# Performance work log

Measured on AMD Instinct MI355X. Metric: run time of the kernel, lower is better.

## Reference

```python
import jax, jax.numpy as jnp
import numpy as np


def setup_inputs() -> dict:
    key = jax.random.key(0)
    k1, k2, k3, k4, k5 = jax.random.split(key, 5)
    B, S, DK, D = 64, 2048, 1024, 1024
    hidden_state = jax.random.normal(k1, (B, D), dtype=jnp.float32)
    encoder_outputs = jax.random.normal(k2, (B, S, DK), dtype=jnp.float32)
    # linear1: in = dim_key + dim*num_layers = 2048, out = dim = 1024
    W1 = jax.random.normal(k3, (D, DK + D), dtype=jnp.float32) * (1.0 / np.sqrt(DK + D))
    b1 = jax.random.normal(k4, (D,), dtype=jnp.float32) * 0.01
    W2 = jax.random.normal(k5, (1, D), dtype=jnp.float32) * (1.0 / np.sqrt(D))
    return {"hidden_state": hidden_state, "encoder_outputs": encoder_outputs,
            "W1": W1, "b1": b1, "W2": W2}


def reference(hidden_state, encoder_outputs, W1, b1, W2):
    # torch: cat([enc, h], -1) @ W1.T  ==  enc @ W1e.T + h @ W1h.T
    # (split avoids materializing the [B,S,DK+D] concat; same math)
    DK = encoder_outputs.shape[-1]
    W1e, W1h = W1[:, :DK], W1[:, DK:]
    # pre: [B, S, D]
    pre = (jnp.einsum('bsk,dk->bsd', encoder_outputs, W1e)
           + jnp.einsum('bm,dm->bd', hidden_state, W1h)[:, None, :]
           + b1)
    e = jnp.einsum('bsd,d->bs', jnp.tanh(pre), W2[0])  # scores [B, S]
    alpha = jax.nn.softmax(e, axis=1)
    context = jnp.einsum('bs,bsk->bk', alpha, encoder_outputs)  # [B, DK]
    return context
```

## Files before the change

kernel.cpp:

```cpp
#include <hip/hip_runtime.h>

typedef __attribute__((ext_vector_type(8))) short short8;
typedef __attribute__((ext_vector_type(4))) float floatx4;

#define M_TOT 131072
#define SEQ   2048
#define NB    8

__device__ __forceinline__ unsigned bf16rne(float x) {
  unsigned u = __float_as_uint(x);
  return (u + 0x7FFFu + ((u >> 16) & 1u)) >> 16;
}

#define GLOAD_LDS16(g, l) __builtin_amdgcn_global_load_lds( \
    (const __attribute__((address_space(1))) unsigned int*)(g), \
    (__attribute__((address_space(3))) unsigned int*)(l), 16, 0, 0)

__global__ __launch_bounds__(256) void convert_enc_kernel(
    const float* __restrict__ in, unsigned int* __restrict__ out)
{
  size_t i = ((size_t)blockIdx.x * 256 + threadIdx.x) * 8;
  float4 a = *(const float4*)(in + i);
  float4 b = *(const float4*)(in + i + 4);
  uint4 o;
  o.x = bf16rne(a.x) | (bf16rne(a.y) << 16);
  o.y = bf16rne(a.z) | (bf16rne(a.w) << 16);
  o.z = bf16rne(b.x) | (bf16rne(b.y) << 16);
  o.w = bf16rne(b.z) | (bf16rne(b.w) << 16);
  *(uint4*)(out + i / 2) = o;
}

__global__ __launch_bounds__(128) void convert_w1e_kernel(
    const float* __restrict__ W1, unsigned int* __restrict__ out)
{
  int d = blockIdx.x;
  int k = threadIdx.x * 8;
  const float* p = W1 + (size_t)d * 2048 + k;
  float4 a = *(const float4*)p;
  float4 b = *(const float4*)(p + 4);
  uint4 o;
  o.x = bf16rne(a.x) | (bf16rne(a.y) << 16);
  o.y = bf16rne(a.z) | (bf16rne(a.w) << 16);
  o.z = bf16rne(b.x) | (bf16rne(b.y) << 16);
  o.w = bf16rne(b.z) | (bf16rne(b.w) << 16);
  *(uint4*)(out + ((size_t)d * 1024 + k) / 2) = o;
}

__global__ __launch_bounds__(256) void hvec_kernel(
    const float* __restrict__ hid, const float* __restrict__ W1,
    const float* __restrict__ b1, float* __restrict__ hvec)
{
  int b = blockIdx.x, g = blockIdx.y;
  int w = threadIdx.x >> 6, lane = threadIdx.x & 63;
  const float* hrow = hid + b * 1024;
  for (int i = 0; i < 16; ++i) {
    int d = g * 64 + w * 16 + i;
    const float* wrow = W1 + (size_t)d * 2048 + 1024;
    float sum = 0.f;
#pragma unroll
    for (int c = 0; c < 4; ++c) {
      int m = c * 256 + lane * 4;
      float4 wv = *(const float4*)(wrow + m);
      float4 hv = *(const float4*)(hrow + m);
      sum += wv.x * hv.x + wv.y * hv.y + wv.z * hv.z + wv.w * hv.w;
    }
#pragma unroll
    for (int msk = 1; msk < 64; msk <<= 1) sum += __shfl_xor(sum, msk);
    if (lane == 0) hvec[b * 1024 + d] = sum + b1[d];
  }
}

__global__ __launch_bounds__(256) void gemm_bf16_kernel(
    const unsigned short* __restrict__ A, const unsigned short* __restrict__ B,
    const float* __restrict__ W2, const float* __restrict__ hvec,
    float* __restrict__ epart)
{
  __shared__ __align__(16) unsigned short Ah[128 * 32];
  __shared__ __align__(16) unsigned short Bh[128 * 32];
  __shared__ float ep[2][128];

  const int tid = threadIdx.x;
  const int lid = blockIdx.x + blockIdx.y * 8;
  const int xcd = lid & 7;
  const int q   = lid >> 3;
  const int mb  = (xcd << 7) + (q >> 3);
  const int nb  = q & 7;
  const int r0 = mb * 128, n0 = nb * 128;
  const int bidx = r0 >> 11;
  const int w = tid >> 6, lane = tid & 63;
  const int wm = w >> 1, wn = w & 1;
  const int lrow = lane & 15, kq = lane >> 4;

  floatx4 acc[4][4];
#pragma unroll
  for (int i = 0; i < 4; ++i)
#pragma unroll
    for (int j = 0; j < 4; ++j)
      acc[i][j] = (floatx4){0.f, 0.f, 0.f, 0.f};

  const unsigned short* aBase = A + (size_t)r0 * 1024;
  const unsigned short* bBase = B + (size_t)n0 * 1024;

  for (int k0 = 0; k0 < 1024; k0 += 32) {
    __syncthreads();
#pragma unroll
    for (int j = 0; j < 2; ++j) {
      int c = tid + j * 256;
      int row = c >> 2, kc = c & 3;
      const unsigned short* ag = aBase + (size_t)row * 1024 + k0 + kc * 8;
      const unsigned short* bg = bBase + (size_t)row * 1024 + k0 + kc * 8;
      int ldsbase = (w * 64 + j * 256) * 8;
      GLOAD_LDS16(ag, &Ah[ldsbase]);
      GLOAD_LDS16(bg, &Bh[ldsbase]);
    }
    __syncthreads();

    short8 af[4], bfm[4];
#pragma unroll
    for (int t4 = 0; t4 < 4; ++t4) {
      af[t4]  = *(const short8*)&Ah[(wm * 64 + t4 * 16 + lrow) * 32 + kq * 8];
      bfm[t4] = *(const short8*)&Bh[(wn * 64 + t4 * 16 + lrow) * 32 + kq * 8];
    }
#pragma unroll
    for (int mt = 0; mt < 4; ++mt)
#pragma unroll
      for (int nt = 0; nt < 4; ++nt)
        acc[mt][nt] = __builtin_amdgcn_mfma_f32_16x16x32_bf16(
            af[mt], bfm[nt], acc[mt][nt], 0, 0, 0);
  }

  float hv[4], w2v[4];
#pragma unroll
  for (int nt = 0; nt < 4; ++nt) {
    int n = n0 + wn * 64 + nt * 16 + lrow;
    hv[nt]  = hvec[bidx * 1024 + n];
    w2v[nt] = W2[n];
  }
#pragma unroll
  for (int mt = 0; mt < 4; ++mt) {
#pragma unroll
    for (int r = 0; r < 4; ++r) {
      float sum = 0.f;
#pragma unroll
      for (int nt = 0; nt < 4; ++nt) {
        float pre = acc[mt][nt][r] + hv[nt];
        float ex = __expf(2.f * pre);
        sum += (1.f - 2.f / (ex + 1.f)) * w2v[nt];
      }
      sum += __shfl_xor(sum, 1);
      sum += __shfl_xor(sum, 2);
      sum += __shfl_xor(sum, 4);
      sum += __shfl_xor(sum, 8);
      if (lrow == 0) ep[wn][wm * 64 + mt * 16 + kq * 4 + r] = sum;
    }
  }
  __syncthreads();
  if (tid < 128)
    epart[(size_t)nb * M_TOT + r0 + tid] = ep[0][tid] + ep[1][tid];
}

__global__ __launch_bounds__(256) void fused_gemm_kernel(
    const float* __restrict__ enc, const float* __restrict__ W1,
    const float* __restrict__ W2, const float* __restrict__ hvec,
    float* __restrict__ epart)
{
  __shared__ __align__(16) unsigned short Ah[128 * 32];
  __shared__ __align__(16) unsigned short Bh[128 * 32];
  __shared__ float ep[2][128];

  const int tid = threadIdx.x;
  const int nb = blockIdx.x, mb = blockIdx.y;
  const int r0 = mb * 128, n0 = nb * 128;
  const int bidx = r0 >> 11;
  const int w = tid >> 6, lane = tid & 63;
  const int wm = w >> 1, wn = w & 1;
  const int lrow = lane & 15, kq = lane >> 4;

  floatx4 acc[4][4];
#pragma unroll
  for (int i = 0; i < 4; ++i)
#pragma unroll
    for (int j = 0; j < 4; ++j)
      acc[i][j] = (floatx4){0.f, 0.f, 0.f, 0.f};

  const int srow = tid >> 3;
  const int scol = (tid & 7) * 4;
  const float* aptr = enc + (size_t)(r0 + srow) * 1024 + scol;
  const float* bptr = W1  + (size_t)(n0 + srow) * 2048 + scol;

  for (int k0 = 0; k0 < 1024; k0 += 32) {
    float4 av[4], bv[4];
#pragma unroll
    for (int j = 0; j < 4; ++j) {
      av[j] = *(const float4*)(aptr + (size_t)(j * 32) * 1024 + k0);
      bv[j] = *(const float4*)(bptr + (size_t)(j * 32) * 2048 + k0);
    }
    __syncthreads();
#pragma unroll
    for (int j = 0; j < 4; ++j) {
      unsigned ax = __float_as_uint(av[j].x), ay = __float_as_uint(av[j].y);
      unsigned az = __float_as_uint(av[j].z), aw = __float_as_uint(av[j].w);
      unsigned a01 = __builtin_amdgcn_perm(ay, ax, 0x07060302u);
      unsigned a23 = __builtin_amdgcn_perm(aw, az, 0x07060302u);
      *(uint2*)&Ah[(tid + j * 256) * 4] = make_uint2(a01, a23);
      unsigned bx = __float_as_uint(bv[j].x), by = __float_as_uint(bv[j].y);
      unsigned bz = __float_as_uint(bv[j].z), bw = __float_as_uint(bv[j].w);
      unsigned b01 = __builtin_amdgcn_perm(by, bx, 0x07060302u);
      unsigned b23 = __builtin_amdgcn_perm(bw, bz, 0x07060302u);
      *(uint2*)&Bh[(tid + j * 256) * 4] = make_uint2(b01, b23);
    }
    __syncthreads();

    short8 af[4], bfm[4];
#pragma unroll
    for (int t4 = 0; t4 < 4; ++t4) {
      af[t4]  = *(const short8*)&Ah[(wm * 64 + t4 * 16 + lrow) * 32 + kq * 8];
      bfm[t4] = *(const short8*)&Bh[(wn * 64 + t4 * 16 + lrow) * 32 + kq * 8];
    }
#pragma unroll
    for (int mt = 0; mt < 4; ++mt)
#pragma unroll
      for (int nt = 0; nt < 4; ++nt)
        acc[mt][nt] = __builtin_amdgcn_mfma_f32_16x16x32_bf16(
            af[mt], bfm[nt], acc[mt][nt], 0, 0, 0);
  }

  float hv[4], w2v[4];
#pragma unroll
  for (int nt = 0; nt < 4; ++nt) {
    int n = n0 + wn * 64 + nt * 16 + lrow;
    hv[nt]  = hvec[bidx * 1024 + n];
    w2v[nt] = W2[n];
  }
#pragma unroll
  for (int mt = 0; mt < 4; ++mt) {
#pragma unroll
    for (int r = 0; r < 4; ++r) {
      float sum = 0.f;
#pragma unroll
      for (int nt = 0; nt < 4; ++nt) {
        float pre = acc[mt][nt][r] + hv[nt];
        float ex = __expf(2.f * pre);
        sum += (1.f - 2.f / (ex + 1.f)) * w2v[nt];
      }
      sum += __shfl_xor(sum, 1);
      sum += __shfl_xor(sum, 2);
      sum += __shfl_xor(sum, 4);
      sum += __shfl_xor(sum, 8);
      if (lrow == 0) ep[wn][wm * 64 + mt * 16 + kq * 4 + r] = sum;
    }
  }
  __syncthreads();
  if (tid < 128)
    epart[(size_t)nb * M_TOT + r0 + tid] = ep[0][tid] + ep[1][tid];
}

__global__ __launch_bounds__(256) void softmax_kernel(
    const float* __restrict__ epart, float* __restrict__ alpha)
{
  int b = blockIdx.x, t = threadIdx.x;
  __shared__ float redmax[4], redsum[4];
  float ev[8];
  float lmax = -1e30f;
#pragma unroll
  for (int j = 0; j < 8; ++j) {
    int s = t + j * 256;
    float sum = 0.f;
#pragma unroll
    for (int p = 0; p < 8; ++p) sum += epart[(size_t)p * M_TOT + b * SEQ + s];
    ev[j] = sum;
    lmax = fmaxf(lmax, sum);
  }
#pragma unroll
  for (int msk = 1; msk < 64; msk <<= 1) lmax = fmaxf(lmax, __shfl_xor(lmax, msk));
  if ((t & 63) == 0) redmax[t >> 6] = lmax;
  __syncthreads();
  float bmax = fmaxf(fmaxf(redmax[0], redmax[1]), fmaxf(redmax[2], redmax[3]));
  float lsum = 0.f;
#pragma unroll
  for (int j = 0; j < 8; ++j) { ev[j] = __expf(ev[j] - bmax); lsum += ev[j]; }
#pragma unroll
  for (int msk = 1; msk < 64; msk <<= 1) lsum += __shfl_xor(lsum, msk);
  if ((t & 63) == 0) redsum[t >> 6] = lsum;
  __syncthreads();
  float inv = 1.f / (redsum[0] + redsum[1] + redsum[2] + redsum[3]);
#pragma unroll
  for (int j = 0; j < 8; ++j) alpha[b * SEQ + t + j * 256] = ev[j] * inv;
}

__global__ __launch_bounds__(256) void context_bf16_kernel(
    const unsigned int* __restrict__ encB, const float* __restrict__ alpha,
    float* __restrict__ out)
{
  __shared__ float red[8][128];
  int b = blockIdx.x, kc = blockIdx.y, t = threadIdx.x;
  int kl = (t & 31) * 4;
  int strip = t >> 5;
  const unsigned int* ep = encB +
      (((size_t)b * SEQ + strip * 256) * 1024 + kc * 128 + kl) / 2;
  const float* ap = alpha + b * SEQ + strip * 256;
  float a0 = 0.f, a1 = 0.f, a2 = 0.f, a3 = 0.f;
#pragma unroll 4
  for (int s = 0; s < 256; ++s) {
    float a = ap[s];
    uint2 v = *(const uint2*)(ep + (size_t)s * 512);
    a0 += a * __uint_as_float(v.x << 16);
    a1 += a * __uint_as_float(v.x & 0xFFFF0000u);
    a2 += a * __uint_as_float(v.y << 16);
    a3 += a * __uint_as_float(v.y & 0xFFFF0000u);
  }
  red[strip][kl + 0] = a0;
  red[strip][kl + 1] = a1;
  red[strip][kl + 2] = a2;
  red[strip][kl + 3] = a3;
  __syncthreads();
  if (t < 128) {
    float s = 0.f;
#pragma unroll
    for (int j = 0; j < 8; ++j) s += red[j][t];
    out[b * 1024 + kc * 128 + t] = s;
  }
}

__global__ __launch_bounds__(256) void context_kernel(
    const float* __restrict__ enc, const float* __restrict__ alpha,
    float* __restrict__ out)
{
  int b = blockIdx.y, sq = blockIdx.z, t = threadIdx.x;
  int k4 = t * 4;
  const float* ep = enc + ((size_t)b * SEQ + sq * 128) * 1024 + k4;
  const float* ap = alpha + b * SEQ + sq * 128;
  float ax = 0.f, ay = 0.f, az = 0.f, aw = 0.f;
#pragma unroll 4
  for (int s = 0; s < 128; ++s) {
    float a = ap[s];
    float4 v = *(const float4*)(ep + (size_t)s * 1024);
    ax += a * v.x; ay += a * v.y; az += a * v.z; aw += a * v.w;
  }
  float* o = out + b * 1024 + k4;
  atomicAdd(o + 0, ax);
  atomicAdd(o + 1, ay);
  atomicAdd(o + 2, az);
  atomicAdd(o + 3, aw);
}

extern "C" void kernel_launch(void* const* d_in, const int* in_sizes, int n_in,
                              void* d_out, int out_size, void* d_ws, size_t ws_size,
                              hipStream_t stream) {
  const float* hid = (const float*)d_in[0];
  const float* enc = (const float*)d_in[1];
  const float* W1  = (const float*)d_in[2];
  const float* b1  = (const float*)d_in[3];
  const float* W2  = (const float*)d_in[4];
  float* out = (float*)d_out;

  float* epart = (float*)d_ws;
  float* alpha = epart + (size_t)NB * M_TOT;
  float* hvec  = alpha + M_TOT;
  size_t small_bytes = ((size_t)NB * M_TOT + M_TOT + 64 * 1024) * 4;
  size_t encB_off = ((small_bytes + 255) / 256) * 256;
  size_t need = encB_off + (size_t)M_TOT * 1024 * 2 + (size_t)1024 * 1024 * 2;

  hvec_kernel<<<dim3(64, 16), 256, 0, stream>>>(hid, W1, b1, hvec);

  if (ws_size >= need) {
    unsigned short* encB = (unsigned short*)((char*)d_ws + encB_off);
    unsigned short* W1eB = encB + (size_t)M_TOT * 1024;
    convert_enc_kernel<<<65536, 256, 0, stream>>>(enc, (unsigned int*)encB);
    convert_w1e_kernel<<<1024, 128, 0, stream>>>(W1, (unsigned int*)W1eB);
    gemm_bf16_kernel<<<dim3(NB, 1024), 256, 0, stream>>>(encB, W1eB, W2, hvec, epart);
    softmax_kernel<<<64, 256, 0, stream>>>(epart, alpha);
    context_bf16_kernel<<<dim3(64, 8), 256, 0, stream>>>((unsigned int*)encB, alpha, out);
  } else {
    hipMemsetAsync(d_out, 0, (size_t)out_size * sizeof(float), stream);
    fused_gemm_kernel<<<dim3(NB, 1024), 256, 0, stream>>>(enc, W1, W2, hvec, epart);
    softmax_kernel<<<64, 256, 0, stream>>>(epart, alpha);
    context_kernel<<<dim3(1, 64, 16), 256, 0, stream>>>(enc, alpha, out);
  }
}
```

Measured before the change: 1.157 ms.

## Use 256x256 bf16 GEMM tiles with 4-stage LDS pipeline and async prefetch

Replaces the 128x128 single-buffered bf16 GEMM with a 512-thread 256x256 tile kernel. It prefetches K-slices two steps ahead into a 4-deep LDS ring using global_load_lds, synchronises with explicit vmcnt waits plus barriers, and raises wave priority around the MFMA blocks. The larger tile halves the N-partials, so softmax is templated to sum 4 partials instead of 8. The aim is more data reuse per global load and overlap of memory latency with MFMA work. The cost is 128KB of LDS per block and higher register pressure with 2 blocks per CU requested.

```diff
diff --git a/kernel.cpp b/kernel.cpp
--- a/kernel.cpp
+++ b/kernel.cpp
@@ -70,65 +70,92 @@
   }
 }
 
-__global__ __launch_bounds__(256) void gemm_bf16_kernel(
+__global__ __launch_bounds__(512, 2) void gemm256_kernel(
     const unsigned short* __restrict__ A, const unsigned short* __restrict__ B,
     const float* __restrict__ W2, const float* __restrict__ hvec,
     float* __restrict__ epart)
 {
-  __shared__ __align__(16) unsigned short Ah[128 * 32];
-  __shared__ __align__(16) unsigned short Bh[128 * 32];
-  __shared__ float ep[2][128];
+  __shared__ __align__(16) unsigned short lds[4][2][8192];
 
   const int tid = threadIdx.x;
-  const int lid = blockIdx.x + blockIdx.y * 8;
-  const int xcd = lid & 7;
-  const int q   = lid >> 3;
-  const int mb  = (xcd << 7) + (q >> 3);
-  const int nb  = q & 7;
-  const int r0 = mb * 128, n0 = nb * 128;
+  const int lid = blockIdx.x;
+  const int xcd = lid & 7, q = lid >> 3;
+  const int mb = xcd * 64 + (q >> 2);
+  const int nb = q & 3;
+  const int r0 = mb * 256, n0 = nb * 256;
   const int bidx = r0 >> 11;
-  const int w = tid >> 6, lane = tid & 63;
-  const int wm = w >> 1, wn = w & 1;
+  const int wid = tid >> 6, lane = tid & 63;
+  const int wm = wid >> 2, wn = wid & 3;
   const int lrow = lane & 15, kq = lane >> 4;
 
-  floatx4 acc[4][4];
-#pragma unroll
-  for (int i = 0; i < 4; ++i)
+  int offA[2], offB[2], dst[2];
+#pragma unroll
+  for (int j = 0; j < 2; ++j) {
+    int c = tid + j * 512;
+    int r = c >> 2, s = c & 3;
+    offA[j] = (r0 + r) * 1024 + s * 8;
+    offB[j] = (n0 + r) * 1024 + s * 8;
+    dst[j] = (wid * 64 + j * 512) * 8;
+  }
+
+  floatx4 acc[8][4];
+#pragma unroll
+  for (int i = 0; i < 8; ++i)
 #pragma unroll
     for (int j = 0; j < 4; ++j)
       acc[i][j] = (floatx4){0.f, 0.f, 0.f, 0.f};
 
-  const unsigned short* aBase = A + (size_t)r0 * 1024;
-  const unsigned short* bBase = B + (size_t)n0 * 1024;
-
-  for (int k0 = 0; k0 < 1024; k0 += 32) {
-    __syncthreads();
-#pragma unroll
-    for (int j = 0; j < 2; ++j) {
-      int c = tid + j * 256;
-      int row = c >> 2, kc = c & 3;
-      const unsigned short* ag = aBase + (size_t)row * 1024 + k0 + kc * 8;
-      const unsigned short* bg = bBase + (size_t)row * 1024 + k0 + kc * 8;
-      int ldsbase = (w * 64 + j * 256) * 8;
-      GLOAD_LDS16(ag, &Ah[ldsbase]);
-      GLOAD_LDS16(bg, &Bh[ldsbase]);
-    }
-    __syncthreads();
-
-    short8 af[4], bfm[4];
-#pragma unroll
-    for (int t4 = 0; t4 < 4; ++t4) {
-      af[t4]  = *(const short8*)&Ah[(wm * 64 + t4 * 16 + lrow) * 32 + kq * 8];
-      bfm[t4] = *(const short8*)&Bh[(wn * 64 + t4 * 16 + lrow) * 32 + kq * 8];
-    }
-#pragma unroll
-    for (int mt = 0; mt < 4; ++mt)
-#pragma unroll
-      for (int nt = 0; nt < 4; ++nt)
-        acc[mt][nt] = __builtin_amdgcn_mfma_f32_16x16x32_bf16(
-            af[mt], bfm[nt], acc[mt][nt], 0, 0, 0);
-  }
-
+#define STAGE_J(T, J) do { \
+    GLOAD_LDS16(A + (size_t)offA[J] + (T) * 32, &lds[(T) & 3][0][dst[J]]); \
+    GLOAD_LDS16(B + (size_t)offB[J] + (T) * 32, &lds[(T) & 3][1][dst[J]]); \
+  } while (0)
+
+  STAGE_J(0, 0); STAGE_J(0, 1);
+  STAGE_J(1, 0); STAGE_J(1, 1);
+
+  const int aB = wm * 4096 + lrow * 32 + kq * 8;
+  const int bB = wn * 2048 + lrow * 32 + kq * 8;
+
+  for (int tt = 0; tt < 8; ++tt) {
+#pragma unroll
+    for (int u = 0; u < 4; ++u) {
+      const int t = tt * 4 + u;
+      const unsigned short* Ah = lds[u][0];
+      const unsigned short* Bh = lds[u][1];
+
+      if (t >= 30) { asm volatile("s_waitcnt vmcnt(0)" ::: "memory"); }
+      else         { asm volatile("s_waitcnt vmcnt(4)" ::: "memory"); }
+      __builtin_amdgcn_s_barrier();
+
+      short8 af[8];
+#pragma unroll
+      for (int mt = 0; mt < 8; ++mt) af[mt] = *(const short8*)&Ah[aB + mt * 512];
+      short8 bf0 = *(const short8*)&Bh[bB];
+      short8 bf1 = *(const short8*)&Bh[bB + 512];
+      if (t < 30) STAGE_J(t + 2, 0);
+      __builtin_amdgcn_s_setprio(1);
+#pragma unroll
+      for (int mt = 0; mt < 8; ++mt) {
+        acc[mt][0] = __builtin_amdgcn_mfma_f32_16x16x32_bf16(af[mt], bf0, acc[mt][0], 0, 0, 0);
+        acc[mt][1] = __builtin_amdgcn_mfma_f32_16x16x32_bf16(af[mt], bf1, acc[mt][1], 0, 0, 0);
+      }
+      __builtin_amdgcn_s_setprio(0);
+      short8 bf2 = *(const short8*)&Bh[bB + 1024];
+      short8 bf3 = *(const short8*)&Bh[bB + 1536];
+      if (t < 30) STAGE_J(t + 2, 1);
+      __builtin_amdgcn_s_setprio(1);
+#pragma unroll
+      for (int mt = 0; mt < 8; ++mt) {
+        acc[mt][2] = __builtin_amdgcn_mfma_f32_16x16x32_bf16(af[mt], bf2, acc[mt][2], 0, 0, 0);
+        acc[mt][3] = __builtin_amdgcn_mfma_f32_16x16x32_bf16(af[mt], bf3, acc[mt][3], 0, 0, 0);
+      }
+      __builtin_amdgcn_s_setprio(0);
+    }
+  }
+#undef STAGE_J
+
+  __syncthreads();
+  float* ep = (float*)&lds[0][0][0];
   float hv[4], w2v[4];
 #pragma unroll
   for (int nt = 0; nt < 4; ++nt) {
@@ -137,7 +164,7 @@
     w2v[nt] = W2[n];
   }
 #pragma unroll
-  for (int mt = 0; mt < 4; ++mt) {
+  for (int mt = 0; mt < 8; ++mt) {
 #pragma unroll
     for (int r = 0; r < 4; ++r) {
       float sum = 0.f;
@@ -151,12 +178,14 @@
       sum += __shfl_xor(sum, 2);
       sum += __shfl_xor(sum, 4);
       sum += __shfl_xor(sum, 8);
-      if (lrow == 0) ep[wn][wm * 64 + mt * 16 + kq * 4 + r] = sum;
-    }
-  }
-  __syncthreads();
-  if (tid < 128)
-    epart[(size_t)nb * M_TOT + r0 + tid] = ep[0][tid] + ep[1][tid];
+      if (lrow == 0) ep[wn * 256 + wm * 128 + mt * 16 + kq * 4 + r] = sum;
+    }
+  }
+  __syncthreads();
+  if (tid < 256) {
+    float s = ep[tid] + ep[256 + tid] + ep[512 + tid] + ep[768 + tid];
+    epart[(size_t)nb * M_TOT + r0 + tid] = s;
+  }
 }
 
 __global__ __launch_bounds__(256) void fused_gemm_kernel(
@@ -255,6 +284,7 @@
     epart[(size_t)nb * M_TOT + r0 + tid] = ep[0][tid] + ep[1][tid];
 }
 
+template<int NP>
 __global__ __launch_bounds__(256) void softmax_kernel(
     const float* __restrict__ epart, float* __restrict__ alpha)
 {
@@ -267,7 +297,7 @@
     int s = t + j * 256;
     float sum = 0.f;
 #pragma unroll
-    for (int p = 0; p < 8; ++p) sum += epart[(size_t)p * M_TOT + b * SEQ + s];
+    for (int p = 0; p < NP; ++p) sum += epart[(size_t)p * M_TOT + b * SEQ + s];
     ev[j] = sum;
     lmax = fmaxf(lmax, sum);
   }
@@ -368,13 +398,13 @@
     unsigned short* W1eB = encB + (size_t)M_TOT * 1024;
     convert_enc_kernel<<<65536, 256, 0, stream>>>(enc, (unsigned int*)encB);
     convert_w1e_kernel<<<1024, 128, 0, stream>>>(W1, (unsigned int*)W1eB);
-    gemm_bf16_kernel<<<dim3(NB, 1024), 256, 0, stream>>>(encB, W1eB, W2, hvec, epart);
-    softmax_kernel<<<64, 256, 0, stream>>>(epart, alpha);
+    gemm256_kernel<<<2048, 512, 0, stream>>>(encB, W1eB, W2, hvec, epart);
+    softmax_kernel<4><<<64, 256, 0, stream>>>(epart, alpha);
     context_bf16_kernel<<<dim3(64, 8), 256, 0, stream>>>((unsigned int*)encB, alpha, out);
   } else {
     hipMemsetAsync(d_out, 0, (size_t)out_size * sizeof(float), stream);
     fused_gemm_kernel<<<dim3(NB, 1024), 256, 0, stream>>>(enc, W1, W2, hvec, epart);
-    softmax_kernel<<<64, 256, 0, stream>>>(epart, alpha);
+    softmax_kernel<8><<<64, 256, 0, stream>>>(epart, alpha);
     context_kernel<<<dim3(1, 64, 16), 256, 0, stream>>>(enc, alpha, out);
   }
 }
```

Result: faster. 1.083 ms (-6.4%).

## Fuse encoder bf16 conversion into GEMM with pipelined fragment-layout W1 loads

Applied to the files above, without the earlier changes.

Removes the separate pass that converted the whole encoder tensor to bf16. The GEMM now loads fp32 encoder rows, converts them in registers with v_cvt_pk_bf16_f32 and stores them to double-buffered LDS. W1e is pre-packed into an MFMA fragment layout and prefetched into a 4-stage LDS ring, with manual waitcnt and setprio. The context pass reads fp32 encoder data directly with 512 threads, and hvec is spread over more blocks. This avoids writing and re-reading a 256MB bf16 copy, but the GEMM and the context pass now each read the full fp32 encoder tensor, and the GEMM does more per-thread conversion work.

```diff
diff --git a/kernel.cpp b/kernel.cpp
--- a/kernel.cpp
+++ b/kernel.cpp
@@ -12,30 +12,22 @@
   return (u + 0x7FFFu + ((u >> 16) & 1u)) >> 16;
 }
 
+__device__ __forceinline__ unsigned cvtpk_bf16(float lo, float hi) {
+  unsigned r;
+  asm("v_cvt_pk_bf16_f32 %0, %1, %2" : "=v"(r) : "v"(lo), "v"(hi));
+  return r;
+}
+
 #define GLOAD_LDS16(g, l) __builtin_amdgcn_global_load_lds( \
     (const __attribute__((address_space(1))) unsigned int*)(g), \
     (__attribute__((address_space(3))) unsigned int*)(l), 16, 0, 0)
 
-__global__ __launch_bounds__(256) void convert_enc_kernel(
-    const float* __restrict__ in, unsigned int* __restrict__ out)
-{
-  size_t i = ((size_t)blockIdx.x * 256 + threadIdx.x) * 8;
-  float4 a = *(const float4*)(in + i);
-  float4 b = *(const float4*)(in + i + 4);
-  uint4 o;
-  o.x = bf16rne(a.x) | (bf16rne(a.y) << 16);
-  o.y = bf16rne(a.z) | (bf16rne(a.w) << 16);
-  o.z = bf16rne(b.x) | (bf16rne(b.y) << 16);
-  o.w = bf16rne(b.z) | (bf16rne(b.w) << 16);
-  *(uint4*)(out + i / 2) = o;
-}
-
-__global__ __launch_bounds__(128) void convert_w1e_kernel(
+__global__ __launch_bounds__(128) void convert_w1e_frag_kernel(
     const float* __restrict__ W1, unsigned int* __restrict__ out)
 {
   int d = blockIdx.x;
-  int k = threadIdx.x * 8;
-  const float* p = W1 + (size_t)d * 2048 + k;
+  int kc = threadIdx.x;
+  const float* p = W1 + (size_t)d * 2048 + kc * 8;
   float4 a = *(const float4*)p;
   float4 b = *(const float4*)(p + 4);
   uint4 o;
@@ -43,7 +35,10 @@
   o.y = bf16rne(a.z) | (bf16rne(a.w) << 16);
   o.z = bf16rne(b.x) | (bf16rne(b.y) << 16);
   o.w = bf16rne(b.z) | (bf16rne(b.w) << 16);
-  *(uint4*)(out + ((size_t)d * 1024 + k) / 2) = o;
+  int nb = d >> 7, f = (d >> 4) & 7, t = kc >> 2;
+  int lane = (d & 15) + ((kc & 3) << 4);
+  size_t chunk = ((size_t)(nb * 32 + t) * 8 + f) * 64 + lane;
+  *(uint4*)(out + chunk * 4) = o;
 }
 
 __global__ __launch_bounds__(256) void hvec_kernel(
@@ -53,8 +48,8 @@
   int b = blockIdx.x, g = blockIdx.y;
   int w = threadIdx.x >> 6, lane = threadIdx.x & 63;
   const float* hrow = hid + b * 1024;
-  for (int i = 0; i < 16; ++i) {
-    int d = g * 64 + w * 16 + i;
+  for (int i = 0; i < 4; ++i) {
+    int d = g * 16 + w * 4 + i;
     const float* wrow = W1 + (size_t)d * 2048 + 1024;
     float sum = 0.f;
 #pragma unroll
@@ -70,26 +65,34 @@
   }
 }
 
-__global__ __launch_bounds__(256) void gemm_bf16_kernel(
-    const unsigned short* __restrict__ A, const unsigned short* __restrict__ B,
+__global__ __launch_bounds__(256, 3) void gemm128_kernel(
+    const float* __restrict__ enc, const unsigned short* __restrict__ Bfrag,
     const float* __restrict__ W2, const float* __restrict__ hvec,
     float* __restrict__ epart)
 {
-  __shared__ __align__(16) unsigned short Ah[128 * 32];
-  __shared__ __align__(16) unsigned short Bh[128 * 32];
-  __shared__ float ep[2][128];
+  __shared__ __align__(16) unsigned short ldsA[2][4096];
+  __shared__ __align__(16) unsigned short ldsB[4][4096];
 
   const int tid = threadIdx.x;
-  const int lid = blockIdx.x + blockIdx.y * 8;
-  const int xcd = lid & 7;
-  const int q   = lid >> 3;
-  const int mb  = (xcd << 7) + (q >> 3);
-  const int nb  = q & 7;
-  const int r0 = mb * 128, n0 = nb * 128;
-  const int bidx = r0 >> 11;
-  const int w = tid >> 6, lane = tid & 63;
-  const int wm = w >> 1, wn = w & 1;
+  const int lid = blockIdx.x;
+  const int xcd = lid & 7, q = lid >> 3;
+  const int mb = xcd * 128 + (q >> 3);
+  const int nb = q & 7;
+  const int r0 = mb * 128;
+  const int bidx = mb >> 4;
+  const int wid = tid >> 6, lane = tid & 63;
+  const int wm = wid >> 1, wn = wid & 1;
   const int lrow = lane & 15, kq = lane >> 4;
+
+  const float* aSrc[2];
+  int aDst[2];
+#pragma unroll
+  for (int j = 0; j < 2; ++j) {
+    int c = tid + j * 256, row = c >> 2, kc = c & 3;
+    aSrc[j] = enc + (size_t)(r0 + row) * 1024 + kc * 8;
+    aDst[j] = ((row >> 4) * 64 + (row & 15) + (kc << 4)) * 8;
+  }
+  const unsigned short* bBase = Bfrag + (size_t)nb * 32 * 4096;
 
   floatx4 acc[4][4];
 #pragma unroll
@@ -98,41 +101,75 @@
     for (int j = 0; j < 4; ++j)
       acc[i][j] = (floatx4){0.f, 0.f, 0.f, 0.f};
 
-  const unsigned short* aBase = A + (size_t)r0 * 1024;
-  const unsigned short* bBase = B + (size_t)n0 * 1024;
-
-  for (int k0 = 0; k0 < 1024; k0 += 32) {
-    __syncthreads();
-#pragma unroll
-    for (int j = 0; j < 2; ++j) {
-      int c = tid + j * 256;
-      int row = c >> 2, kc = c & 3;
-      const unsigned short* ag = aBase + (size_t)row * 1024 + k0 + kc * 8;
-      const unsigned short* bg = bBase + (size_t)row * 1024 + k0 + kc * 8;
-      int ldsbase = (w * 64 + j * 256) * 8;
-      GLOAD_LDS16(ag, &Ah[ldsbase]);
-      GLOAD_LDS16(bg, &Bh[ldsbase]);
-    }
-    __syncthreads();
-
-    short8 af[4], bfm[4];
-#pragma unroll
-    for (int t4 = 0; t4 < 4; ++t4) {
-      af[t4]  = *(const short8*)&Ah[(wm * 64 + t4 * 16 + lrow) * 32 + kq * 8];
-      bfm[t4] = *(const short8*)&Bh[(wn * 64 + t4 * 16 + lrow) * 32 + kq * 8];
-    }
-#pragma unroll
-    for (int mt = 0; mt < 4; ++mt)
+  float4 aR[2][2];
+#pragma unroll
+  for (int j = 0; j < 2; ++j) {
+    aR[j][0] = *(const float4*)(aSrc[j]);
+    aR[j][1] = *(const float4*)(aSrc[j] + 4);
+  }
+  GLOAD_LDS16(bBase + tid * 8,         &ldsB[0][wid * 512]);
+  GLOAD_LDS16(bBase + (tid + 256) * 8, &ldsB[0][wid * 512 + 2048]);
+
+  const int aOff = wm * 2048 + lane * 8;
+  const int bOff = wn * 2048 + lane * 8;
+
+  for (int tt = 0; tt < 8; ++tt) {
+#pragma unroll
+    for (int u = 0; u < 4; ++u) {
+      const int t = tt * 4 + u;
+      const int sA = u & 1;
+      const int sB = u;
+      const int sBn = (u + 1) & 3;
+#pragma unroll
+      for (int j = 0; j < 2; ++j) {
+        uint4 o;
+        o.x = cvtpk_bf16(aR[j][0].x, aR[j][0].y);
+        o.y = cvtpk_bf16(aR[j][0].z, aR[j][0].w);
+        o.z = cvtpk_bf16(aR[j][1].x, aR[j][1].y);
+        o.w = cvtpk_bf16(aR[j][1].z, aR[j][1].w);
+        *(uint4*)&ldsA[sA][aDst[j]] = o;
+      }
+      const bool more = (u < 3) || (tt < 7);
+      if (more) {
+#pragma unroll
+        for (int j = 0; j < 2; ++j) {
+          aR[j][0] = *(const float4*)(aSrc[j] + (t + 1) * 32);
+          aR[j][1] = *(const float4*)(aSrc[j] + (t + 1) * 32 + 4);
+        }
+        GLOAD_LDS16(bBase + (size_t)(t + 1) * 4096 + tid * 8,
+                    &ldsB[sBn][wid * 512]);
+        GLOAD_LDS16(bBase + (size_t)(t + 1) * 4096 + (tid + 256) * 8,
+                    &ldsB[sBn][wid * 512 + 2048]);
+        asm volatile("s_waitcnt vmcnt(6)" ::: "memory");
+      } else {
+        asm volatile("s_waitcnt vmcnt(0)" ::: "memory");
+      }
+      asm volatile("s_waitcnt lgkmcnt(0)" ::: "memory");
+      __builtin_amdgcn_s_barrier();
+      short8 af[4], bf[4];
+#pragma unroll
+      for (int mt = 0; mt < 4; ++mt)
+        af[mt] = *(const short8*)&ldsA[sA][aOff + mt * 512];
 #pragma unroll
       for (int nt = 0; nt < 4; ++nt)
-        acc[mt][nt] = __builtin_amdgcn_mfma_f32_16x16x32_bf16(
-            af[mt], bfm[nt], acc[mt][nt], 0, 0, 0);
-  }
-
+        bf[nt] = *(const short8*)&ldsB[sB][bOff + nt * 512];
+      __builtin_amdgcn_s_setprio(1);
+#pragma unroll
+      for (int mt = 0; mt < 4; ++mt)
+#pragma unroll
+        for (int nt = 0; nt < 4; ++nt)
+          acc[mt][nt] = __builtin_amdgcn_mfma_f32_16x16x32_bf16(
+              af[mt], bf[nt], acc[mt][nt], 0, 0, 0);
+      __builtin_amdgcn_s_setprio(0);
+    }
+  }
+
+  __syncthreads();
+  float* ep = (float*)&ldsA[0][0];
   float hv[4], w2v[4];
 #pragma unroll
   for (int nt = 0; nt < 4; ++nt) {
-    int n = n0 + wn * 64 + nt * 16 + lrow;
+    int n = nb * 128 + wn * 64 + nt * 16 + lrow;
     hv[nt]  = hvec[bidx * 1024 + n];
     w2v[nt] = W2[n];
   }
@@ -151,12 +188,12 @@
       sum += __shfl_xor(sum, 2);
       sum += __shfl_xor(sum, 4);
       sum += __shfl_xor(sum, 8);
-      if (lrow == 0) ep[wn][wm * 64 + mt * 16 + kq * 4 + r] = sum;
+      if (lrow == 0) ep[wn * 128 + wm * 64 + mt * 16 + kq * 4 + r] = sum;
     }
   }
   __syncthreads();
   if (tid < 128)
-    epart[(size_t)nb * M_TOT + r0 + tid] = ep[0][tid] + ep[1][tid];
+    epart[(size_t)nb * M_TOT + r0 + tid] = ep[tid] + ep[128 + tid];
 }
 
 __global__ __launch_bounds__(256) void fused_gemm_kernel(
@@ -288,26 +325,22 @@
   for (int j = 0; j < 8; ++j) alpha[b * SEQ + t + j * 256] = ev[j] * inv;
 }
 
-__global__ __launch_bounds__(256) void context_bf16_kernel(
-    const unsigned int* __restrict__ encB, const float* __restrict__ alpha,
+__global__ __launch_bounds__(512) void context_f32_kernel(
+    const float* __restrict__ enc, const float* __restrict__ alpha,
     float* __restrict__ out)
 {
-  __shared__ float red[8][128];
+  __shared__ float red[16][128];
   int b = blockIdx.x, kc = blockIdx.y, t = threadIdx.x;
   int kl = (t & 31) * 4;
   int strip = t >> 5;
-  const unsigned int* ep = encB +
-      (((size_t)b * SEQ + strip * 256) * 1024 + kc * 128 + kl) / 2;
-  const float* ap = alpha + b * SEQ + strip * 256;
+  const float* ep = enc + ((size_t)b * SEQ + strip * 128) * 1024 + kc * 128 + kl;
+  const float* ap = alpha + b * SEQ + strip * 128;
   float a0 = 0.f, a1 = 0.f, a2 = 0.f, a3 = 0.f;
 #pragma unroll 4
-  for (int s = 0; s < 256; ++s) {
+  for (int s = 0; s < 128; ++s) {
     float a = ap[s];
-    uint2 v = *(const uint2*)(ep + (size_t)s * 512);
-    a0 += a * __uint_as_float(v.x << 16);
-    a1 += a * __uint_as_float(v.x & 0xFFFF0000u);
-    a2 += a * __uint_as_float(v.y << 16);
-    a3 += a * __uint_as_float(v.y & 0xFFFF0000u);
+    float4 v = *(const float4*)(ep + (size_t)s * 1024);
+    a0 += a * v.x; a1 += a * v.y; a2 += a * v.z; a3 += a * v.w;
   }
   red[strip][kl + 0] = a0;
   red[strip][kl + 1] = a1;
@@ -317,7 +350,7 @@
   if (t < 128) {
     float s = 0.f;
 #pragma unroll
-    for (int j = 0; j < 8; ++j) s += red[j][t];
+    for (int j = 0; j < 16; ++j) s += red[j][t];
     out[b * 1024 + kc * 128 + t] = s;
   }
 }
@@ -358,19 +391,17 @@
   float* alpha = epart + (size_t)NB * M_TOT;
   float* hvec  = alpha + M_TOT;
   size_t small_bytes = ((size_t)NB * M_TOT + M_TOT + 64 * 1024) * 4;
-  size_t encB_off = ((small_bytes + 255) / 256) * 256;
-  size_t need = encB_off + (size_t)M_TOT * 1024 * 2 + (size_t)1024 * 1024 * 2;
-
-  hvec_kernel<<<dim3(64, 16), 256, 0, stream>>>(hid, W1, b1, hvec);
+  size_t w1eb_off = ((small_bytes + 255) / 256) * 256;
+  size_t need = w1eb_off + (size_t)1024 * 1024 * 2;
+
+  hvec_kernel<<<dim3(64, 64), 256, 0, stream>>>(hid, W1, b1, hvec);
 
   if (ws_size >= need) {
-    unsigned short* encB = (unsigned short*)((char*)d_ws + encB_off);
-    unsigned short* W1eB = encB + (size_t)M_TOT * 1024;
-    convert_enc_kernel<<<65536, 256, 0, stream>>>(enc, (unsigned int*)encB);
-    convert_w1e_kernel<<<1024, 128, 0, stream>>>(W1, (unsigned int*)W1eB);
-    gemm_bf16_kernel<<<dim3(NB, 1024), 256, 0, stream>>>(encB, W1eB, W2, hvec, epart);
+    unsigned short* W1eB = (unsigned short*)((char*)d_ws + w1eb_off);
+    convert_w1e_frag_kernel<<<1024, 128, 0, stream>>>(W1, (unsigned int*)W1eB);
+    gemm128_kernel<<<8192, 256, 0, stream>>>(enc, W1eB, W2, hvec, epart);
     softmax_kernel<<<64, 256, 0, stream>>>(epart, alpha);
-    context_bf16_kernel<<<dim3(64, 8), 256, 0, stream>>>((unsigned int*)encB, alpha, out);
+    context_f32_kernel<<<dim3(64, 8), 512, 0, stream>>>(enc, alpha, out);
   } else {
     hipMemsetAsync(d_out, 0, (size_t)out_size * sizeof(float), stream);
     fused_gemm_kernel<<<dim3(NB, 1024), 256, 0, stream>>>(enc, W1, W2, hvec, epart);
```

New measurement: 1.130 ms. 1.02x faster.
